# Optimization experiments

Hardware: AMD Instinct MI355X
Metric: run time of the kernel (lower is better)

## Reference

```python
import jax, jax.numpy as jnp
import numpy as np

B, T, D, H = 4, 1024, 1024, 16


def setup_inputs() -> dict:
    key = jax.random.key(0)
    ks = jax.random.split(key, 8)
    s = 0.02
    return {
        "query": jax.random.normal(ks[0], (B, T, D), jnp.float32),
        "key": jax.random.normal(ks[1], (B, T, D), jnp.float32),
        "values": jax.random.normal(ks[2], (B, T, D), jnp.float32),
        "Wq": jax.random.normal(ks[3], (D, D), jnp.float32) * s,
        "bq": jnp.zeros((D,), jnp.float32),
        "Wv": jax.random.normal(ks[4], (D, D), jnp.float32) * s,
        "bv": jnp.zeros((D,), jnp.float32),
        "Wo": jax.random.normal(ks[5], (D, D), jnp.float32) * s,
        "bo": jnp.zeros((D,), jnp.float32),
        "gammas": jax.random.normal(ks[6], (H,), jnp.float32) * 0.1,
        "ln_g": jnp.ones((D,), jnp.float32),
        "ln_b": jnp.zeros((D,), jnp.float32),
    }


def _layer(query, key, values, Wq, bq, Wv, bv, Wo, bo, gammas, ln_g, ln_b):
    b, t, d = query.shape
    h = gammas.shape[0]
    dk = d // h

    def proj(x, W, bias):  # torch Linear: x @ W.T + b, then split heads -> (b,h,t,dk)
        y = jnp.einsum('btd,ed->bte', x, W) + bias
        return y.reshape(b, t, h, dk).transpose(0, 2, 1, 3)

    q = proj(query, Wq, bq)
    k = proj(key, Wq, bq)   # kq_same=True
    v = proj(values, Wv, bv)

    scores = jnp.einsum('bhqd,bhkd->bhqk', q, k) / np.float32(np.sqrt(dk))
    idx = jnp.arange(t)
    pos = jnp.abs(idx[:, None] - idx[None, :]).astype(scores.dtype)  # |i-j|, (t,t)
    mask = idx[:, None] > idx[None, :]  # strict lower tril (peek_cur=False)
    neg = jnp.asarray(-1e32, scores.dtype)

    # gamma time-effect (computed without grad in original)
    s_ = jax.nn.softmax(jnp.where(mask, scores, neg), axis=-1)
    distcum = jnp.cumsum(s_, axis=-1)
    disttotal = jnp.sum(s_, axis=-1, keepdims=True)
    dist = jnp.sqrt(jnp.clip((disttotal - distcum) * pos, 0.0, None))
    dist = jax.lax.stop_gradient(dist)
    gamma_eff = -jnp.abs(gammas)[None, :, None, None]  # (1,h,1,1)
    total_effect = jnp.clip(jnp.exp(dist * gamma_eff), 1e-5, 1e5)
    scores = scores * total_effect

    p = jax.nn.softmax(jnp.where(mask, scores, neg), axis=-1)
    p = jnp.where(mask, p, 0.0)
    # maxout rescale (maxout=True since peek_cur=False)
    scale = jnp.minimum(1.0 / jnp.max(p, axis=-1, keepdims=True), 5.0)
    p = p * scale

    out = jnp.einsum('bhqk,bhkd->bhqd', p, v)
    concat = out.transpose(0, 2, 1, 3).reshape(b, t, d)
    attn_out = jnp.einsum('btd,ed->bte', concat, Wo) + bo

    x = query + attn_out  # residual (dropout is identity in eval)
    mu = jnp.mean(x, axis=-1, keepdims=True)
    var = jnp.var(x, axis=-1, keepdims=True)
    return (x - mu) / jnp.sqrt(var + 1e-5) * ln_g + ln_b


def reference(query, key, values, Wq, bq, Wv, bv, Wo, bo, gammas, ln_g, ln_b):
    return _layer(query, key, values, Wq, bq, Wv, bv, Wo, bo, gammas, ln_g, ln_b)
```

## Files before the change

kernel.cpp:

```cpp
#include <hip/hip_runtime.h>
#include <hip/hip_bf16.h>
#include <stdint.h>


typedef unsigned short ushort_t;
typedef __attribute__((ext_vector_type(8))) short short8;
typedef __attribute__((ext_vector_type(8))) unsigned short u16x8;
typedef __attribute__((ext_vector_type(4))) float f32x4;
typedef __attribute__((ext_vector_type(4))) unsigned short u16x4;
typedef __attribute__((ext_vector_type(2))) unsigned short u16x2;

#define GLB_CAST(p) ((const __attribute__((address_space(1))) void*)(p))
#define LDS_CAST(p) ((__attribute__((address_space(3))) void*)(p))

#if __has_builtin(__builtin_amdgcn_exp2f)
#define EXP2F(x) __builtin_amdgcn_exp2f(x)
#else
#define EXP2F(x) exp2f(x)
#endif

#define LOG2E 1.44269504f

__device__ __forceinline__ float b2f(ushort_t u) {
  union { unsigned int i; float f; } x; x.i = ((unsigned int)u) << 16; return x.f;
}
__device__ __forceinline__ ushort_t f2b(float f) {
  __hip_bfloat16 h = __float2bfloat16(f);
  return *reinterpret_cast<ushort_t*>(&h);
}
__device__ __forceinline__ float wave_sum(float v) {
  #pragma unroll
  for (int d = 32; d > 0; d >>= 1) v += __shfl_xor(v, d);
  return v;
}

__global__ void conv6_f32_bf16(const float* __restrict__ s0, const float* __restrict__ s1,
                               const float* __restrict__ s2, const float* __restrict__ s3,
                               const float* __restrict__ s4, const float* __restrict__ s5,
                               ushort_t* __restrict__ d0, ushort_t* __restrict__ d1,
                               ushort_t* __restrict__ d2, ushort_t* __restrict__ d3,
                               ushort_t* __restrict__ d4, ushort_t* __restrict__ d5,
                               int n4tok, int n4w) {
  const int y = blockIdx.y;
  const float* srcs[6] = {s0, s1, s2, s3, s4, s5};
  ushort_t*    dsts[6] = {d0, d1, d2, d3, d4, d5};
  const int n4 = (y < 3) ? n4tok : n4w;
  int i = blockIdx.x * blockDim.x + threadIdx.x;
  if (i < n4) {
    const float4 v = reinterpret_cast<const float4*>(srcs[y])[i];
    u16x4 o;
    o[0] = f2b(v.x); o[1] = f2b(v.y); o[2] = f2b(v.z); o[3] = f2b(v.w);
    reinterpret_cast<u16x4*>(dsts[y])[i] = o;
  }
}

__device__ __forceinline__ void gemm_core(const ushort_t* __restrict__ A,
                                          const ushort_t* __restrict__ Bt,
                                          int m0, int n0,
                                          ushort_t* As, ushort_t* Bs,
                                          f32x4 (&acc)[4][4]) {
  const int tid = threadIdx.x, lane = tid & 63;
  const int wid = tid >> 6;
  const int wr = (wid >> 1) * 64, wc = (wid & 1) * 64;
  for (int k0 = 0; k0 < 1024; k0 += 32) {
    #pragma unroll
    for (int it = 0; it < 2; ++it) {
      const int idx = tid * 8 + it * 2048;
      const int r = idx >> 5, kk = idx & 31;
      __builtin_amdgcn_global_load_lds(GLB_CAST(&A[(size_t)(m0 + r) * 1024 + k0 + kk]),
                                       LDS_CAST(&As[idx]), 16, 0, 0);
      __builtin_amdgcn_global_load_lds(GLB_CAST(&Bt[(size_t)(n0 + r) * 1024 + k0 + kk]),
                                       LDS_CAST(&Bs[idx]), 16, 0, 0);
    }
    __syncthreads();
    short8 af[4], bfv[4];
    #pragma unroll
    for (int m = 0; m < 4; ++m)
      af[m] = *reinterpret_cast<const short8*>(&As[(wr + m * 16 + (lane & 15)) * 32 + (lane >> 4) * 8]);
    #pragma unroll
    for (int n = 0; n < 4; ++n)
      bfv[n] = *reinterpret_cast<const short8*>(&Bs[(wc + n * 16 + (lane & 15)) * 32 + (lane >> 4) * 8]);
    #pragma unroll
    for (int m = 0; m < 4; ++m)
      #pragma unroll
      for (int n = 0; n < 4; ++n)
        acc[m][n] = __builtin_amdgcn_mfma_f32_16x16x32_bf16(af[m], bfv[n], acc[m][n], 0, 0, 0);
    __syncthreads();
  }
}

__global__ __launch_bounds__(256) void gemm_proj(
    const ushort_t* __restrict__ qb, const ushort_t* __restrict__ kb, const ushort_t* __restrict__ vb,
    const ushort_t* __restrict__ Wqb, const ushort_t* __restrict__ Wvb,
    const float* __restrict__ bq, const float* __restrict__ bvv,
    ushort_t* __restrict__ Qh, ushort_t* __restrict__ Kh, ushort_t* __restrict__ Vt) {
  __shared__ ushort_t As[128 * 32], Bs[128 * 32];
  const ushort_t* A; const ushort_t* Bt; const float* bias;
  if (blockIdx.z == 0)      { A = qb; Bt = Wqb; bias = bq;  }
  else if (blockIdx.z == 1) { A = kb; Bt = Wqb; bias = bq;  }
  else                      { A = vb; Bt = Wvb; bias = bvv; }
  const int m0 = blockIdx.y * 128, n0 = blockIdx.x * 128;
  f32x4 zero = {0.f, 0.f, 0.f, 0.f};
  f32x4 acc[4][4];
  #pragma unroll
  for (int m = 0; m < 4; ++m)
    #pragma unroll
    for (int n = 0; n < 4; ++n) acc[m][n] = zero;
  gemm_core(A, Bt, m0, n0, As, Bs, acc);
  const int lane = threadIdx.x & 63, wid = threadIdx.x >> 6;
  const int wr = (wid >> 1) * 64, wc = (wid & 1) * 64;
  if (blockIdx.z == 2) {
    #pragma unroll
    for (int m = 0; m < 4; ++m)
      #pragma unroll
      for (int n = 0; n < 4; ++n) {
        const int rowb = m0 + wr + m * 16 + (lane >> 4) * 4;
        const int col  = n0 + wc + n * 16 + (lane & 15);
        u16x4 pk;
        #pragma unroll
        for (int r4 = 0; r4 < 4; ++r4) pk[r4] = f2b(acc[m][n][r4] + bias[col]);
        const int bi = rowb >> 10, t = rowb & 1023;
        *reinterpret_cast<u16x4*>(
            &Vt[((size_t)(bi * 16 + (col >> 6)) * 64 + (col & 63)) * 1024 + t]) = pk;
      }
  } else {
    ushort_t* dst = (blockIdx.z == 0) ? Qh : Kh;
    #pragma unroll
    for (int m = 0; m < 4; ++m)
      #pragma unroll
      for (int n = 0; n < 4; ++n)
        #pragma unroll
        for (int r4 = 0; r4 < 4; ++r4) {
          const int row = m0 + wr + m * 16 + (lane >> 4) * 4 + r4;
          const int col = n0 + wc + n * 16 + (lane & 15);
          const float v = acc[m][n][r4] + bias[col];
          const int bi = row >> 10, t = row & 1023, h = col >> 6, dd = col & 63;
          dst[((size_t)(bi * 16 + h) * 1024 + t) * 64 + dd] = f2b(v);
        }
  }
}

__global__ __launch_bounds__(256) void gemm_out(
    const ushort_t* __restrict__ A, const ushort_t* __restrict__ Bt,
    const float* __restrict__ bias, const float* __restrict__ resid,
    float* __restrict__ dstF) {
  __shared__ ushort_t As[128 * 32], Bs[128 * 32];
  const int m0 = blockIdx.y * 128, n0 = blockIdx.x * 128;
  f32x4 zero = {0.f, 0.f, 0.f, 0.f};
  f32x4 acc[4][4];
  #pragma unroll
  for (int m = 0; m < 4; ++m)
    #pragma unroll
    for (int n = 0; n < 4; ++n) acc[m][n] = zero;
  gemm_core(A, Bt, m0, n0, As, Bs, acc);
  const int lane = threadIdx.x & 63, wid = threadIdx.x >> 6;
  const int wr = (wid >> 1) * 64, wc = (wid & 1) * 64;
  #pragma unroll
  for (int m = 0; m < 4; ++m)
    #pragma unroll
    for (int n = 0; n < 4; ++n)
      #pragma unroll
      for (int r4 = 0; r4 < 4; ++r4) {
        const int row = m0 + wr + m * 16 + (lane >> 4) * 4 + r4;
        const int col = n0 + wc + n * 16 + (lane & 15);
        const size_t o = (size_t)row * 1024 + col;
        dstF[o] = acc[m][n][r4] + bias[col] + resid[o];
      }
}

template<int CH>
__device__ __forceinline__ void load_row(const ushort_t* __restrict__ Row, float (&s)[CH]) {
  constexpr int W = (CH % 8 == 0) ? 8 : (CH % 4 == 0) ? 4 : (CH % 2 == 0) ? 2 : 1;
  #pragma unroll
  for (int b = 0; b < CH / W; ++b) {
    if constexpr (W == 8) {
      const u16x8 t = *reinterpret_cast<const u16x8*>(&Row[b * 8]);
      #pragma unroll
      for (int e = 0; e < 8; ++e) s[b * 8 + e] = b2f(t[e]);
    } else if constexpr (W == 4) {
      const u16x4 t = *reinterpret_cast<const u16x4*>(&Row[b * 4]);
      #pragma unroll
      for (int e = 0; e < 4; ++e) s[b * 4 + e] = b2f(t[e]);
    } else if constexpr (W == 2) {
      const u16x2 t = *reinterpret_cast<const u16x2*>(&Row[b * 2]);
      s[b * 2] = b2f(t[0]); s[b * 2 + 1] = b2f(t[1]);
    } else {
      s[b] = b2f(Row[b]);
    }
  }
}

template<int CH>
__device__ __forceinline__ void store_row(ushort_t* __restrict__ Row,
                                          const float (&p)[CH], const float sc) {
  constexpr int W = (CH % 8 == 0) ? 8 : (CH % 4 == 0) ? 4 : (CH % 2 == 0) ? 2 : 1;
  #pragma unroll
  for (int b = 0; b < CH / W; ++b) {
    if constexpr (W == 8) {
      u16x8 o;
      #pragma unroll
      for (int e = 0; e < 8; ++e) o[e] = f2b(p[b * 8 + e] * sc);
      *reinterpret_cast<u16x8*>(&Row[b * 8]) = o;
    } else if constexpr (W == 4) {
      u16x4 o;
      #pragma unroll
      for (int e = 0; e < 4; ++e) o[e] = f2b(p[b * 4 + e] * sc);
      *reinterpret_cast<u16x4*>(&Row[b * 4]) = o;
    } else if constexpr (W == 2) {
      u16x2 o;
      o[0] = f2b(p[b * 2] * sc); o[1] = f2b(p[b * 2 + 1] * sc);
      *reinterpret_cast<u16x2*>(&Row[b * 2]) = o;
    } else {
      Row[b] = f2b(p[b] * sc);
    }
  }
}

template<int CH>
__device__ __forceinline__ void phase_b(ushort_t* __restrict__ Sb, const int i0,
                                        const int w, const int lane, const float gamx) {
  const int c0 = CH * lane;
  for (int rr = 0; rr < 4; ++rr) {
    const int r = w * 4 + rr;
    const int i = i0 + r;
    ushort_t* __restrict__ Row = &Sb[r * 1032 + c0];
    if (i == 0) {
      #pragma unroll
      for (int e = 0; e < CH; ++e) Row[e] = 0;
      continue;
    }
    const int nact = min(max(i - c0, 0), CH);
    float s[CH], ev[CH];
    load_row<CH>(Row, s);
    float run = 0.f;
    #pragma unroll
    for (int e = 0; e < CH; ++e) {
      s[e] = (e < nact) ? s[e] * LOG2E : -__builtin_inff();
      ev[e] = EXP2F(s[e]);
      run += ev[e];
    }
    float v = run;
    #pragma unroll
    for (int d = 1; d < 64; d <<= 1) {
      const float t = __shfl_down(v, d);
      v += (lane + d < 64) ? t : 0.f;
    }
    const float Z1 = __shfl(v, 0);
    float run2 = v - run;
    const float g2 = -gamx * rsqrtf(Z1);
    const float posb = (float)(i - c0);
    float z2 = 0.f, mm = 0.f;
    #pragma unroll
    for (int e = CH - 1; e >= 0; --e) {
      const float t = fmaxf(run2 * (posb - (float)e), 0.f);
      run2 += ev[e];
      const float eff = fmaxf(EXP2F(g2 * sqrtf(t)), 1e-5f);
      const float p = EXP2F(s[e] * eff);
      ev[e] = p;
      z2 += p;
      mm = fmaxf(mm, p);
    }
    #pragma unroll
    for (int d = 32; d > 0; d >>= 1) {
      z2 += __shfl_xor(z2, d);
      mm = fmaxf(mm, __shfl_xor(mm, d));
    }
    const float sc = fminf(1.f / mm, 5.f / z2);
    store_row<CH>(Row, ev, sc);
  }
}

__global__ __launch_bounds__(256, 4) void attn_kernel(
    const ushort_t* __restrict__ Qh, const ushort_t* __restrict__ Kh,
    const ushort_t* __restrict__ Vt, const float* __restrict__ gammas,
    ushort_t* __restrict__ concat) {
  __shared__ __align__(16) ushort_t Sb[16 * 1032];
  __shared__ __align__(16) ushort_t Qs[16 * 72];
  const int tid = threadIdx.x, lane = tid & 63, w = tid >> 6;
  const int flat = blockIdx.x + (blockIdx.y << 6);
  const int bh = ((flat & 7) << 3) | (flat >> 9);
  const int i0 = (63 - ((flat >> 3) & 63)) << 4;
  const int bi = bh >> 4, h = bh & 15;
  const size_t base = (size_t)bh * (1024 * 64);

  {
    const int r = tid >> 4, d = (tid & 15) * 4;
    *reinterpret_cast<u16x4*>(&Qs[r * 72 + d]) =
        *reinterpret_cast<const u16x4*>(&Qh[base + (size_t)(i0 + r) * 64 + d]);
  }
  __syncthreads();

  const int upper = i0 + 16;
  for (int nt = 0; nt < 16; ++nt) {
    const int colbase = (nt * 4 + w) * 16;
    if (colbase >= upper) break;
    f32x4 acc = {0.f, 0.f, 0.f, 0.f};
    #pragma unroll
    for (int kt = 0; kt < 2; ++kt) {
      const short8 a = *reinterpret_cast<const short8*>(
          &Qs[(lane & 15) * 72 + kt * 32 + (lane >> 4) * 8]);
      const short8 bb = *reinterpret_cast<const short8*>(
          &Kh[base + (size_t)(colbase + (lane & 15)) * 64 + kt * 32 + (lane >> 4) * 8]);
      acc = __builtin_amdgcn_mfma_f32_16x16x32_bf16(a, bb, acc, 0, 0, 0);
    }
    const int j = colbase + (lane & 15);
    #pragma unroll
    for (int r4 = 0; r4 < 4; ++r4) {
      const int rf = (lane >> 4) * 4 + r4;
      Sb[rf * 1032 + j] = f2b(acc[r4] * 0.125f);
    }
  }
  __syncthreads();

  const float gamx = fabsf(gammas[h]) * LOG2E;
  const int chp = (upper + 63) >> 6;
  switch (chp) {
    case 1:           phase_b<1 >(Sb, i0, w, lane, gamx); break;
    case 2:           phase_b<2 >(Sb, i0, w, lane, gamx); break;
    case 3: case 4:   phase_b<4 >(Sb, i0, w, lane, gamx); break;
    case 5: case 6:   phase_b<6 >(Sb, i0, w, lane, gamx); break;
    case 7: case 8:   phase_b<8 >(Sb, i0, w, lane, gamx); break;
    case 9: case 10:  phase_b<10>(Sb, i0, w, lane, gamx); break;
    case 11: case 12: phase_b<12>(Sb, i0, w, lane, gamx); break;
    case 13: case 14: phase_b<14>(Sb, i0, w, lane, gamx); break;
    default:          phase_b<16>(Sb, i0, w, lane, gamx); break;
  }
  __syncthreads();

  {
    const int d0 = w * 16;
    const int arow = lane & 15;
    const ushort_t* Prow = &Sb[arow * 1032];
    const ushort_t* Vrow = Vt + base + (size_t)(d0 + arow) * 1024;
    const int kmax = (upper + 31) & ~31;
    f32x4 acc = {0.f, 0.f, 0.f, 0.f};
    for (int k0 = 0; k0 < kmax; k0 += 32) {
      const short8 a = *reinterpret_cast<const short8*>(&Prow[k0 + (lane >> 4) * 8]);
      const short8 bb = *reinterpret_cast<const short8*>(&Vrow[k0 + (lane >> 4) * 8]);
      acc = __builtin_amdgcn_mfma_f32_16x16x32_bf16(a, bb, acc, 0, 0, 0);
    }
    #pragma unroll
    for (int r4 = 0; r4 < 4; ++r4) {
      const int row = (lane >> 4) * 4 + r4;
      const int i = i0 + row;
      concat[((size_t)(bi * 1024 + i)) * 1024 + h * 64 + d0 + arow] = f2b(acc[r4]);
    }
  }
}

__global__ __launch_bounds__(256) void ln_kernel(const float* __restrict__ x,
                                                 const float* __restrict__ g,
                                                 const float* __restrict__ bb,
                                                 float* __restrict__ out) {
  const int row = blockIdx.x, tid = threadIdx.x, lane = tid & 63, w = tid >> 6;
  const float4 v = reinterpret_cast<const float4*>(x + (size_t)row * 1024)[tid];
  float s = v.x + v.y + v.z + v.w;
  float q = v.x * v.x + v.y * v.y + v.z * v.z + v.w * v.w;
  s = wave_sum(s); q = wave_sum(q);
  __shared__ float ps[4], pq[4];
  if (lane == 0) { ps[w] = s; pq[w] = q; }
  __syncthreads();
  const float ts = ps[0] + ps[1] + ps[2] + ps[3];
  const float tq = pq[0] + pq[1] + pq[2] + pq[3];
  const float mu = ts * (1.f / 1024.f);
  const float inv = rsqrtf(tq * (1.f / 1024.f) - mu * mu + 1e-5f);
  const float4 gv = reinterpret_cast<const float4*>(g)[tid];
  const float4 bv = reinterpret_cast<const float4*>(bb)[tid];
  float4 o;
  o.x = (v.x - mu) * inv * gv.x + bv.x;
  o.y = (v.y - mu) * inv * gv.y + bv.y;
  o.z = (v.z - mu) * inv * gv.z + bv.z;
  o.w = (v.w - mu) * inv * gv.w + bv.w;
  reinterpret_cast<float4*>(out + (size_t)row * 1024)[tid] = o;
}

extern "C" void kernel_launch(void* const* d_in, const int* in_sizes, int n_in,
                              void* d_out, int out_size, void* d_ws, size_t ws_size,
                              hipStream_t stream) {
  (void)in_sizes; (void)n_in; (void)out_size; (void)ws_size;
  const float* query  = (const float*)d_in[0];
  const float* key    = (const float*)d_in[1];
  const float* values = (const float*)d_in[2];
  const float* Wq     = (const float*)d_in[3];
  const float* bq     = (const float*)d_in[4];
  const float* Wv     = (const float*)d_in[5];
  const float* bv     = (const float*)d_in[6];
  const float* Wo     = (const float*)d_in[7];
  const float* bo     = (const float*)d_in[8];
  const float* gammas = (const float*)d_in[9];
  const float* ln_g   = (const float*)d_in[10];
  const float* ln_b   = (const float*)d_in[11];
  float* out = (float*)d_out;

  const size_t NT = 4096ull * 1024;
  const size_t NW = 1024ull * 1024;
  char* p = (char*)d_ws;
  ushort_t* qb  = (ushort_t*)p; p += NT * 2;
  ushort_t* kb  = (ushort_t*)p; p += NT * 2;
  ushort_t* vb  = (ushort_t*)p; p += NT * 2;
  ushort_t* Wqb = (ushort_t*)p; p += NW * 2;
  ushort_t* Wvb = (ushort_t*)p; p += NW * 2;
  ushort_t* Wob = (ushort_t*)p; p += NW * 2;
  ushort_t* Qh  = (ushort_t*)p; p += NT * 2;
  ushort_t* Kh  = (ushort_t*)p; p += NT * 2;
  ushort_t* Vt  = (ushort_t*)p; p += NT * 2;
  ushort_t* concat = vb;
  float*    xbuf   = (float*)qb;

  conv6_f32_bf16<<<dim3(4096, 6), 256, 0, stream>>>(
      query, key, values, Wq, Wv, Wo, qb, kb, vb, Wqb, Wvb, Wob,
      (int)(NT / 4), (int)(NW / 4));

  gemm_proj<<<dim3(8, 32, 3), 256, 0, stream>>>(qb, kb, vb, Wqb, Wvb, bq, bv, Qh, Kh, Vt);
  attn_kernel<<<dim3(64, 64), 256, 0, stream>>>(Qh, Kh, Vt, gammas, concat);
  gemm_out<<<dim3(8, 32), 256, 0, stream>>>(concat, Wob, bo, query, xbuf);
  ln_kernel<<<4096, 256, 0, stream>>>(xbuf, ln_g, ln_b, out);
}
```

Baseline: 173.5 us.

## Share Wq tile across Q and K projections in a fused projection kernel

Replaces the three-way projection GEMM with one kernel in which a block computes both the Q and K projections for the same 64x128 tile. The Wq B-tile is loaded into LDS once and reused for both inputs, cutting weight loads. Tiles shrink from 128x128 to 64 rows, giving 1024 blocks with launch_bounds occupancy hint 2, which improves parallelism at the cost of lower per-block compute intensity. The V projection blocks form the other half of the grid, so Q/K blocks do twice the MFMA work of V blocks and the load is imbalanced.

```diff
diff --git a/kernel.cpp b/kernel.cpp
--- a/kernel.cpp
+++ b/kernel.cpp
@@ -54,6 +54,122 @@
   }
 }
 
+__global__ __launch_bounds__(256, 2) void gemm_proj_all(
+    const ushort_t* __restrict__ qb, const ushort_t* __restrict__ kb,
+    const ushort_t* __restrict__ vb, const ushort_t* __restrict__ Wqb,
+    const ushort_t* __restrict__ Wvb, const float* __restrict__ bq,
+    const float* __restrict__ bvv,
+    ushort_t* __restrict__ Qh, ushort_t* __restrict__ Kh, ushort_t* __restrict__ Vt) {
+  __shared__ ushort_t As0[64 * 32], As1[64 * 32], Bs[128 * 32];
+  const int tid = threadIdx.x, lane = tid & 63, wid = tid >> 6;
+  const int wr = (wid >> 1) * 32, wc = (wid & 1) * 64;
+  const int flat = blockIdx.x;
+  const f32x4 zero = {0.f, 0.f, 0.f, 0.f};
+  if (flat < 512) {
+    const int m0 = (flat >> 3) * 64, n0 = (flat & 7) * 128;
+    f32x4 accq[2][4], acck[2][4];
+    #pragma unroll
+    for (int m = 0; m < 2; ++m)
+      #pragma unroll
+      for (int n = 0; n < 4; ++n) { accq[m][n] = zero; acck[m][n] = zero; }
+    for (int k0 = 0; k0 < 1024; k0 += 32) {
+      {
+        const int idx = tid * 8, r = idx >> 5, kk = idx & 31;
+        __builtin_amdgcn_global_load_lds(GLB_CAST(&qb[(size_t)(m0 + r) * 1024 + k0 + kk]),
+                                         LDS_CAST(&As0[idx]), 16, 0, 0);
+        __builtin_amdgcn_global_load_lds(GLB_CAST(&kb[(size_t)(m0 + r) * 1024 + k0 + kk]),
+                                         LDS_CAST(&As1[idx]), 16, 0, 0);
+      }
+      #pragma unroll
+      for (int it = 0; it < 2; ++it) {
+        const int idx = tid * 8 + it * 2048, r = idx >> 5, kk = idx & 31;
+        __builtin_amdgcn_global_load_lds(GLB_CAST(&Wqb[(size_t)(n0 + r) * 1024 + k0 + kk]),
+                                         LDS_CAST(&Bs[idx]), 16, 0, 0);
+      }
+      __syncthreads();
+      short8 aq[2], ak[2], bf[4];
+      #pragma unroll
+      for (int m = 0; m < 2; ++m) {
+        aq[m] = *reinterpret_cast<const short8*>(&As0[(wr + m * 16 + (lane & 15)) * 32 + (lane >> 4) * 8]);
+        ak[m] = *reinterpret_cast<const short8*>(&As1[(wr + m * 16 + (lane & 15)) * 32 + (lane >> 4) * 8]);
+      }
+      #pragma unroll
+      for (int n = 0; n < 4; ++n)
+        bf[n] = *reinterpret_cast<const short8*>(&Bs[(wc + n * 16 + (lane & 15)) * 32 + (lane >> 4) * 8]);
+      #pragma unroll
+      for (int m = 0; m < 2; ++m)
+        #pragma unroll
+        for (int n = 0; n < 4; ++n) {
+          accq[m][n] = __builtin_amdgcn_mfma_f32_16x16x32_bf16(aq[m], bf[n], accq[m][n], 0, 0, 0);
+          acck[m][n] = __builtin_amdgcn_mfma_f32_16x16x32_bf16(ak[m], bf[n], acck[m][n], 0, 0, 0);
+        }
+      __syncthreads();
+    }
+    #pragma unroll
+    for (int m = 0; m < 2; ++m)
+      #pragma unroll
+      for (int n = 0; n < 4; ++n)
+        #pragma unroll
+        for (int r4 = 0; r4 < 4; ++r4) {
+          const int row = m0 + wr + m * 16 + (lane >> 4) * 4 + r4;
+          const int col = n0 + wc + n * 16 + (lane & 15);
+          const float bb = bq[col];
+          const int bi = row >> 10, t = row & 1023, h = col >> 6, dd = col & 63;
+          const size_t o = ((size_t)(bi * 16 + h) * 1024 + t) * 64 + dd;
+          Qh[o] = f2b(accq[m][n][r4] + bb);
+          Kh[o] = f2b(acck[m][n][r4] + bb);
+        }
+  } else {
+    const int f2 = flat - 512;
+    const int m0 = (f2 >> 3) * 64, n0 = (f2 & 7) * 128;
+    f32x4 acc[2][4];
+    #pragma unroll
+    for (int m = 0; m < 2; ++m)
+      #pragma unroll
+      for (int n = 0; n < 4; ++n) acc[m][n] = zero;
+    for (int k0 = 0; k0 < 1024; k0 += 32) {
+      {
+        const int idx = tid * 8, r = idx >> 5, kk = idx & 31;
+        __builtin_amdgcn_global_load_lds(GLB_CAST(&vb[(size_t)(m0 + r) * 1024 + k0 + kk]),
+                                         LDS_CAST(&As0[idx]), 16, 0, 0);
+      }
+      #pragma unroll
+      for (int it = 0; it < 2; ++it) {
+        const int idx = tid * 8 + it * 2048, r = idx >> 5, kk = idx & 31;
+        __builtin_amdgcn_global_load_lds(GLB_CAST(&Wvb[(size_t)(n0 + r) * 1024 + k0 + kk]),
+                                         LDS_CAST(&Bs[idx]), 16, 0, 0);
+      }
+      __syncthreads();
+      short8 av[2], bf[4];
+      #pragma unroll
+      for (int m = 0; m < 2; ++m)
+        av[m] = *reinterpret_cast<const short8*>(&As0[(wr + m * 16 + (lane & 15)) * 32 + (lane >> 4) * 8]);
+      #pragma unroll
+      for (int n = 0; n < 4; ++n)
+        bf[n] = *reinterpret_cast<const short8*>(&Bs[(wc + n * 16 + (lane & 15)) * 32 + (lane >> 4) * 8]);
+      #pragma unroll
+      for (int m = 0; m < 2; ++m)
+        #pragma unroll
+        for (int n = 0; n < 4; ++n)
+          acc[m][n] = __builtin_amdgcn_mfma_f32_16x16x32_bf16(av[m], bf[n], acc[m][n], 0, 0, 0);
+      __syncthreads();
+    }
+    #pragma unroll
+    for (int m = 0; m < 2; ++m)
+      #pragma unroll
+      for (int n = 0; n < 4; ++n) {
+        const int rowb = m0 + wr + m * 16 + (lane >> 4) * 4;
+        const int col  = n0 + wc + n * 16 + (lane & 15);
+        u16x4 pk;
+        #pragma unroll
+        for (int r4 = 0; r4 < 4; ++r4) pk[r4] = f2b(acc[m][n][r4] + bvv[col]);
+        const int bi = rowb >> 10, t = rowb & 1023;
+        *reinterpret_cast<u16x4*>(
+            &Vt[((size_t)(bi * 16 + (col >> 6)) * 64 + (col & 63)) * 1024 + t]) = pk;
+      }
+  }
+}
+
 __device__ __forceinline__ void gemm_core(const ushort_t* __restrict__ A,
                                           const ushort_t* __restrict__ Bt,
                                           int m0, int n0,
@@ -86,57 +202,6 @@
       for (int n = 0; n < 4; ++n)
         acc[m][n] = __builtin_amdgcn_mfma_f32_16x16x32_bf16(af[m], bfv[n], acc[m][n], 0, 0, 0);
     __syncthreads();
-  }
-}
-
-__global__ __launch_bounds__(256) void gemm_proj(
-    const ushort_t* __restrict__ qb, const ushort_t* __restrict__ kb, const ushort_t* __restrict__ vb,
-    const ushort_t* __restrict__ Wqb, const ushort_t* __restrict__ Wvb,
-    const float* __restrict__ bq, const float* __restrict__ bvv,
-    ushort_t* __restrict__ Qh, ushort_t* __restrict__ Kh, ushort_t* __restrict__ Vt) {
-  __shared__ ushort_t As[128 * 32], Bs[128 * 32];
-  const ushort_t* A; const ushort_t* Bt; const float* bias;
-  if (blockIdx.z == 0)      { A = qb; Bt = Wqb; bias = bq;  }
-  else if (blockIdx.z == 1) { A = kb; Bt = Wqb; bias = bq;  }
-  else                      { A = vb; Bt = Wvb; bias = bvv; }
-  const int m0 = blockIdx.y * 128, n0 = blockIdx.x * 128;
-  f32x4 zero = {0.f, 0.f, 0.f, 0.f};
-  f32x4 acc[4][4];
-  #pragma unroll
-  for (int m = 0; m < 4; ++m)
-    #pragma unroll
-    for (int n = 0; n < 4; ++n) acc[m][n] = zero;
-  gemm_core(A, Bt, m0, n0, As, Bs, acc);
-  const int lane = threadIdx.x & 63, wid = threadIdx.x >> 6;
-  const int wr = (wid >> 1) * 64, wc = (wid & 1) * 64;
-  if (blockIdx.z == 2) {
-    #pragma unroll
-    for (int m = 0; m < 4; ++m)
-      #pragma unroll
-      for (int n = 0; n < 4; ++n) {
-        const int rowb = m0 + wr + m * 16 + (lane >> 4) * 4;
-        const int col  = n0 + wc + n * 16 + (lane & 15);
-        u16x4 pk;
-        #pragma unroll
-        for (int r4 = 0; r4 < 4; ++r4) pk[r4] = f2b(acc[m][n][r4] + bias[col]);
-        const int bi = rowb >> 10, t = rowb & 1023;
-        *reinterpret_cast<u16x4*>(
-            &Vt[((size_t)(bi * 16 + (col >> 6)) * 64 + (col & 63)) * 1024 + t]) = pk;
-      }
-  } else {
-    ushort_t* dst = (blockIdx.z == 0) ? Qh : Kh;
-    #pragma unroll
-    for (int m = 0; m < 4; ++m)
-      #pragma unroll
-      for (int n = 0; n < 4; ++n)
-        #pragma unroll
-        for (int r4 = 0; r4 < 4; ++r4) {
-          const int row = m0 + wr + m * 16 + (lane >> 4) * 4 + r4;
-          const int col = n0 + wc + n * 16 + (lane & 15);
-          const float v = acc[m][n][r4] + bias[col];
-          const int bi = row >> 10, t = row & 1023, h = col >> 6, dd = col & 63;
-          dst[((size_t)(bi * 16 + h) * 1024 + t) * 64 + dd] = f2b(v);
-        }
   }
 }
 
@@ -411,7 +476,7 @@
       query, key, values, Wq, Wv, Wo, qb, kb, vb, Wqb, Wvb, Wob,
       (int)(NT / 4), (int)(NW / 4));
 
-  gemm_proj<<<dim3(8, 32, 3), 256, 0, stream>>>(qb, kb, vb, Wqb, Wvb, bq, bv, Qh, Kh, Vt);
+  gemm_proj_all<<<dim3(1024), 256, 0, stream>>>(qb, kb, vb, Wqb, Wvb, bq, bv, Qh, Kh, Vt);
   attn_kernel<<<dim3(64, 64), 256, 0, stream>>>(Qh, Kh, Vt, gammas, concat);
   gemm_out<<<dim3(8, 32), 256, 0, stream>>>(concat, Wob, bo, query, xbuf);
   ln_kernel<<<4096, 256, 0, stream>>>(xbuf, ln_g, ln_b, out);
```

Measured after the change: 176.2 us. About the same (+1.5%).

## Fuse fp32-to-bf16 activation conversion into projection GEMM A-tile loads

Applied to the files above, without the earlier changes.

Removes the separate conversion pass over query/key/values. The projection GEMM now reads fp32 activations directly, converts them to bf16 in registers and writes them to LDS, while weights are still pre-converted by a smaller three-tensor kernel. This saves writing and re-reading 24MB of bf16 intermediates, but the A tile is now loaded synchronously through registers instead of async global_load_lds. Each A tile is also reconverted by every column block (8x redundant conversion) and fetched as fp32, doubling the A read bytes.

```diff
diff --git a/kernel.cpp b/kernel.cpp
--- a/kernel.cpp
+++ b/kernel.cpp
@@ -34,43 +34,48 @@
   return v;
 }
 
-__global__ void conv6_f32_bf16(const float* __restrict__ s0, const float* __restrict__ s1,
-                               const float* __restrict__ s2, const float* __restrict__ s3,
-                               const float* __restrict__ s4, const float* __restrict__ s5,
+__global__ void conv3_f32_bf16(const float* __restrict__ s0, const float* __restrict__ s1,
+                               const float* __restrict__ s2,
                                ushort_t* __restrict__ d0, ushort_t* __restrict__ d1,
-                               ushort_t* __restrict__ d2, ushort_t* __restrict__ d3,
-                               ushort_t* __restrict__ d4, ushort_t* __restrict__ d5,
-                               int n4tok, int n4w) {
-  const int y = blockIdx.y;
-  const float* srcs[6] = {s0, s1, s2, s3, s4, s5};
-  ushort_t*    dsts[6] = {d0, d1, d2, d3, d4, d5};
-  const int n4 = (y < 3) ? n4tok : n4w;
+                               ushort_t* __restrict__ d2, int n4) {
+  const float* src = (blockIdx.y == 0) ? s0 : (blockIdx.y == 1) ? s1 : s2;
+  ushort_t*    dst = (blockIdx.y == 0) ? d0 : (blockIdx.y == 1) ? d1 : d2;
   int i = blockIdx.x * blockDim.x + threadIdx.x;
   if (i < n4) {
-    const float4 v = reinterpret_cast<const float4*>(srcs[y])[i];
+    const float4 v = reinterpret_cast<const float4*>(src)[i];
     u16x4 o;
     o[0] = f2b(v.x); o[1] = f2b(v.y); o[2] = f2b(v.z); o[3] = f2b(v.w);
-    reinterpret_cast<u16x4*>(dsts[y])[i] = o;
-  }
-}
-
-__device__ __forceinline__ void gemm_core(const ushort_t* __restrict__ A,
-                                          const ushort_t* __restrict__ Bt,
-                                          int m0, int n0,
-                                          ushort_t* As, ushort_t* Bs,
-                                          f32x4 (&acc)[4][4]) {
+    reinterpret_cast<u16x4*>(dst)[i] = o;
+  }
+}
+
+__device__ __forceinline__ void gemm_core_f32A(const float* __restrict__ A,
+                                               const ushort_t* __restrict__ Bt,
+                                               int m0, int n0,
+                                               ushort_t* As, ushort_t* Bs,
+                                               f32x4 (&acc)[4][4]) {
   const int tid = threadIdx.x, lane = tid & 63;
   const int wid = tid >> 6;
   const int wr = (wid >> 1) * 64, wc = (wid & 1) * 64;
+  const int ar = tid >> 1, ak = (tid & 1) * 16;
   for (int k0 = 0; k0 < 1024; k0 += 32) {
     #pragma unroll
     for (int it = 0; it < 2; ++it) {
       const int idx = tid * 8 + it * 2048;
       const int r = idx >> 5, kk = idx & 31;
-      __builtin_amdgcn_global_load_lds(GLB_CAST(&A[(size_t)(m0 + r) * 1024 + k0 + kk]),
-                                       LDS_CAST(&As[idx]), 16, 0, 0);
       __builtin_amdgcn_global_load_lds(GLB_CAST(&Bt[(size_t)(n0 + r) * 1024 + k0 + kk]),
                                        LDS_CAST(&Bs[idx]), 16, 0, 0);
+    }
+    {
+      const float4* src = reinterpret_cast<const float4*>(&A[(size_t)(m0 + ar) * 1024 + k0 + ak]);
+      const float4 v0 = src[0], v1 = src[1], v2 = src[2], v3 = src[3];
+      u16x8 lo, hi;
+      lo[0] = f2b(v0.x); lo[1] = f2b(v0.y); lo[2] = f2b(v0.z); lo[3] = f2b(v0.w);
+      lo[4] = f2b(v1.x); lo[5] = f2b(v1.y); lo[6] = f2b(v1.z); lo[7] = f2b(v1.w);
+      hi[0] = f2b(v2.x); hi[1] = f2b(v2.y); hi[2] = f2b(v2.z); hi[3] = f2b(v2.w);
+      hi[4] = f2b(v3.x); hi[5] = f2b(v3.y); hi[6] = f2b(v3.z); hi[7] = f2b(v3.w);
+      *reinterpret_cast<u16x8*>(&As[ar * 32 + ak]) = lo;
+      *reinterpret_cast<u16x8*>(&As[ar * 32 + ak + 8]) = hi;
     }
     __syncthreads();
     short8 af[4], bfv[4];
@@ -90,15 +95,15 @@
 }
 
 __global__ __launch_bounds__(256) void gemm_proj(
-    const ushort_t* __restrict__ qb, const ushort_t* __restrict__ kb, const ushort_t* __restrict__ vb,
+    const float* __restrict__ qf, const float* __restrict__ kf, const float* __restrict__ vf,
     const ushort_t* __restrict__ Wqb, const ushort_t* __restrict__ Wvb,
     const float* __restrict__ bq, const float* __restrict__ bvv,
     ushort_t* __restrict__ Qh, ushort_t* __restrict__ Kh, ushort_t* __restrict__ Vt) {
   __shared__ ushort_t As[128 * 32], Bs[128 * 32];
-  const ushort_t* A; const ushort_t* Bt; const float* bias;
-  if (blockIdx.z == 0)      { A = qb; Bt = Wqb; bias = bq;  }
-  else if (blockIdx.z == 1) { A = kb; Bt = Wqb; bias = bq;  }
-  else                      { A = vb; Bt = Wvb; bias = bvv; }
+  const float* A; const ushort_t* Bt; const float* bias;
+  if (blockIdx.z == 0)      { A = qf; Bt = Wqb; bias = bq;  }
+  else if (blockIdx.z == 1) { A = kf; Bt = Wqb; bias = bq;  }
+  else                      { A = vf; Bt = Wvb; bias = bvv; }
   const int m0 = blockIdx.y * 128, n0 = blockIdx.x * 128;
   f32x4 zero = {0.f, 0.f, 0.f, 0.f};
   f32x4 acc[4][4];
@@ -106,7 +111,7 @@
   for (int m = 0; m < 4; ++m)
     #pragma unroll
     for (int n = 0; n < 4; ++n) acc[m][n] = zero;
-  gemm_core(A, Bt, m0, n0, As, Bs, acc);
+  gemm_core_f32A(A, Bt, m0, n0, As, Bs, acc);
   const int lane = threadIdx.x & 63, wid = threadIdx.x >> 6;
   const int wr = (wid >> 1) * 64, wc = (wid & 1) * 64;
   if (blockIdx.z == 2) {
@@ -137,6 +142,41 @@
           const int bi = row >> 10, t = row & 1023, h = col >> 6, dd = col & 63;
           dst[((size_t)(bi * 16 + h) * 1024 + t) * 64 + dd] = f2b(v);
         }
+  }
+}
+
+__device__ __forceinline__ void gemm_core(const ushort_t* __restrict__ A,
+                                          const ushort_t* __restrict__ Bt,
+                                          int m0, int n0,
+                                          ushort_t* As, ushort_t* Bs,
+                                          f32x4 (&acc)[4][4]) {
+  const int tid = threadIdx.x, lane = tid & 63;
+  const int wid = tid >> 6;
+  const int wr = (wid >> 1) * 64, wc = (wid & 1) * 64;
+  for (int k0 = 0; k0 < 1024; k0 += 32) {
+    #pragma unroll
+    for (int it = 0; it < 2; ++it) {
+      const int idx = tid * 8 + it * 2048;
+      const int r = idx >> 5, kk = idx & 31;
+      __builtin_amdgcn_global_load_lds(GLB_CAST(&A[(size_t)(m0 + r) * 1024 + k0 + kk]),
+                                       LDS_CAST(&As[idx]), 16, 0, 0);
+      __builtin_amdgcn_global_load_lds(GLB_CAST(&Bt[(size_t)(n0 + r) * 1024 + k0 + kk]),
+                                       LDS_CAST(&Bs[idx]), 16, 0, 0);
+    }
+    __syncthreads();
+    short8 af[4], bfv[4];
+    #pragma unroll
+    for (int m = 0; m < 4; ++m)
+      af[m] = *reinterpret_cast<const short8*>(&As[(wr + m * 16 + (lane & 15)) * 32 + (lane >> 4) * 8]);
+    #pragma unroll
+    for (int n = 0; n < 4; ++n)
+      bfv[n] = *reinterpret_cast<const short8*>(&Bs[(wc + n * 16 + (lane & 15)) * 32 + (lane >> 4) * 8]);
+    #pragma unroll
+    for (int m = 0; m < 4; ++m)
+      #pragma unroll
+      for (int n = 0; n < 4; ++n)
+        acc[m][n] = __builtin_amdgcn_mfma_f32_16x16x32_bf16(af[m], bfv[n], acc[m][n], 0, 0, 0);
+    __syncthreads();
   }
 }
 
@@ -395,23 +435,18 @@
   const size_t NT = 4096ull * 1024;
   const size_t NW = 1024ull * 1024;
   char* p = (char*)d_ws;
-  ushort_t* qb  = (ushort_t*)p; p += NT * 2;
-  ushort_t* kb  = (ushort_t*)p; p += NT * 2;
-  ushort_t* vb  = (ushort_t*)p; p += NT * 2;
-  ushort_t* Wqb = (ushort_t*)p; p += NW * 2;
-  ushort_t* Wvb = (ushort_t*)p; p += NW * 2;
-  ushort_t* Wob = (ushort_t*)p; p += NW * 2;
-  ushort_t* Qh  = (ushort_t*)p; p += NT * 2;
-  ushort_t* Kh  = (ushort_t*)p; p += NT * 2;
-  ushort_t* Vt  = (ushort_t*)p; p += NT * 2;
-  ushort_t* concat = vb;
-  float*    xbuf   = (float*)qb;
-
-  conv6_f32_bf16<<<dim3(4096, 6), 256, 0, stream>>>(
-      query, key, values, Wq, Wv, Wo, qb, kb, vb, Wqb, Wvb, Wob,
-      (int)(NT / 4), (int)(NW / 4));
-
-  gemm_proj<<<dim3(8, 32, 3), 256, 0, stream>>>(qb, kb, vb, Wqb, Wvb, bq, bv, Qh, Kh, Vt);
+  ushort_t* Wqb    = (ushort_t*)p; p += NW * 2;
+  ushort_t* Wvb    = (ushort_t*)p; p += NW * 2;
+  ushort_t* Wob    = (ushort_t*)p; p += NW * 2;
+  ushort_t* Qh     = (ushort_t*)p; p += NT * 2;
+  ushort_t* Kh     = (ushort_t*)p; p += NT * 2;
+  ushort_t* Vt     = (ushort_t*)p; p += NT * 2;
+  ushort_t* concat = (ushort_t*)p; p += NT * 2;
+  float*    xbuf   = (float*)p;    p += NT * 4;
+
+  conv3_f32_bf16<<<dim3(1024, 3), 256, 0, stream>>>(Wq, Wv, Wo, Wqb, Wvb, Wob, (int)(NW / 4));
+
+  gemm_proj<<<dim3(8, 32, 3), 256, 0, stream>>>(query, key, values, Wqb, Wvb, bq, bv, Qh, Kh, Vt);
   attn_kernel<<<dim3(64, 64), 256, 0, stream>>>(Qh, Kh, Vt, gammas, concat);
   gemm_out<<<dim3(8, 32), 256, 0, stream>>>(concat, Wob, bo, query, xbuf);
   ln_kernel<<<4096, 256, 0, stream>>>(xbuf, ln_g, ln_b, out);
```

Result: slower. 189.3 us (+9.1%).
